# Optimization experiments

Measured on AMD Instinct MI355X. Metric: run time of the kernel, lower is better.

## Reference

```python
import jax, jax.numpy as jnp
import numpy as np

LMAX = 4
S2_DIM = (LMAX + 1) ** 2                                  # 25: s2 irreps, mul 1 per l
SO3_DIM = sum((2 * l + 1) ** 2 for l in range(LMAX + 1))  # 165: so3 irreps, mul 2l+1 per l
B = 2048
F_S2, F_SO3 = 1, 16
N_S2_KERNEL = 48      # s2_healpix_grid(rec_level=1)
N_SO3_KERNEL = 192    # so3_near_identity_grid()
N_ACT_GRID = 4000     # SO3Activation resolution=10, aspect_ratio=2 -> 20x10x20, flattened
N_EVAL = 4608         # so3_healpix_grid(rec_level=2): 192 pixels x 24 gamma


def setup_inputs() -> dict:
    ks = jax.random.split(jax.random.key(0), 7)
    return {
        "x": jax.random.normal(ks[0], (B, F_S2, S2_DIM), jnp.float32),
        "w_s2": jax.random.normal(ks[1], (F_S2, F_SO3, N_S2_KERNEL), jnp.float32),
        "Y": jax.random.normal(ks[2], (N_S2_KERNEL, S2_DIM), jnp.float32),
        "w_so3": jax.random.normal(ks[3], (F_SO3, 1, N_SO3_KERNEL), jnp.float32),
        "D_kernel": jax.random.normal(ks[4], (N_SO3_KERNEL, SO3_DIM), jnp.float32),
        "D_act": jax.random.normal(ks[5], (N_ACT_GRID, SO3_DIM), jnp.float32),
        "eval_wigners": jax.random.normal(ks[6], (SO3_DIM, N_EVAL), jnp.float32) / np.sqrt(SO3_DIM),
    }


def _s2_to_so3_linear(x, psi):
    # e3nn o3.Linear(s2_irreps -> so3_irreps, f_in, f_out, external weights)
    # x:   [B, f_in, 25]  (mul 1 per degree l)
    # psi: [f_in, f_out, 25] ; column l^2+j is the weight to output-multiplicity j of degree l
    f_in, f_out = psi.shape[0], psi.shape[1]
    out, s = [], 0
    for l in range(LMAX + 1):
        d = 2 * l + 1
        x_l = x[..., s:s + d]                       # [B, f_in, d]
        p_l = psi[..., s:s + d]                     # [f_in, f_out, d] (j = out-mul idx)
        o = jnp.einsum('bxm,xyj->byjm', x_l, p_l) / np.sqrt(f_in)
        out.append(o.reshape(x.shape[0], f_out, d * d))
        s += d
    return jnp.concatenate(out, axis=-1)            # [B, f_out, 165]


def _so3_to_so3_linear(x, psi):
    # e3nn o3.Linear(so3_irreps -> so3_irreps, f_in, f_out, external weights)
    # x:   [B, f_in, 165] ; psi: [f_in, f_out, 165]
    f_in, f_out = psi.shape[0], psi.shape[1]
    out, s = [], 0
    for l in range(LMAX + 1):
        d = 2 * l + 1
        x_l = x[..., s:s + d * d].reshape(x.shape[0], f_in, d, d)   # [B,f_in,u,m]
        p_l = psi[..., s:s + d * d].reshape(f_in, f_out, d, d)      # [f_in,f_out,u,v]
        o = jnp.einsum('bxum,xyuv->byvm', x_l, p_l) / np.sqrt(f_in * d)
        out.append(o.reshape(x.shape[0], f_out, d * d))
        s += d * d
    return jnp.concatenate(out, axis=-1)            # [B, f_out, 165]


def _forward(x, w_s2, Y, w_so3, D_kernel, D_act, eval_wigners):
    # --- S2Convolution: kernel = SH-transform of grid weights, then irrep-wise linear
    psi1 = jnp.einsum('ni,xyn->xyi', Y, w_s2) / np.sqrt(N_S2_KERNEL)     # [1,16,25]
    h = _s2_to_so3_linear(x, psi1)                                        # [B,16,165]
    # --- SO3Activation: Fourier -> SO(3) grid -> relu -> Fourier
    g = jnp.einsum('bfi,gi->bfg', h, D_act) / np.sqrt(SO3_DIM)            # [B,16,4000]
    g = jax.nn.relu(g)
    h = jnp.einsum('bfg,gi->bfi', g, D_act) * (np.sqrt(SO3_DIM) / N_ACT_GRID)
    # --- SO3Convolution
    psi2 = jnp.einsum('ni,xyn->xyi', D_kernel, w_so3) / np.sqrt(N_SO3_KERNEL)  # [16,1,165]
    harmonics = _so3_to_so3_linear(h, psi2)                               # [B,1,165]
    # --- compute_probabilities: matmul with eval Wigner-D basis + softmax over grid
    probs = jax.nn.softmax(jnp.einsum('bfi,ie->be', harmonics, eval_wigners), axis=1)  # [B,4608]
    # --- top-k masking: zero out everything below the 5th-highest prob of sample 0
    fifth = jax.lax.top_k(probs, 5)[0][0, 4]
    probs = jnp.where(probs < fifth, 0.0, probs)
    return harmonics, probs


def reference(x, w_s2, Y, w_so3, D_kernel, D_act, eval_wigners):
    return _forward(x, w_s2, Y, w_so3, D_kernel, D_act, eval_wigners)
```

## Files before the change

kernel.cpp:

```cpp
#include <hip/hip_runtime.h>

typedef short bf16x8 __attribute__((ext_vector_type(8)));
typedef float f32x16 __attribute__((ext_vector_type(16)));
typedef int   i32x4  __attribute__((ext_vector_type(4)));

#define INV_SQRT165 0.07784989441615349f
#define FINAL_SCALE 0.0032113081446662823f
#define ZERO16 ((f32x16){0.f,0.f,0.f,0.f,0.f,0.f,0.f,0.f,0.f,0.f,0.f,0.f,0.f,0.f,0.f,0.f})

__device__ __forceinline__ unsigned short f2bf(float f) {
  unsigned int u = __builtin_bit_cast(unsigned int, f);
  unsigned int r = (u + 0x7FFFu + ((u >> 16) & 1u)) >> 16;
  return (unsigned short)r;
}
__device__ __forceinline__ float bf2f(unsigned short h) {
  unsigned int u = ((unsigned int)h) << 16;
  return __builtin_bit_cast(float, u);
}
__device__ __forceinline__ unsigned int pack_bf2(float lo, float hi) {
  return ((unsigned int)f2bf(hi) << 16) | (unsigned int)f2bf(lo);
}

__device__ __forceinline__ void gl_lds16(const void* g, void* l) {
  __builtin_amdgcn_global_load_lds(
      (const __attribute__((address_space(1))) unsigned int*)(unsigned long long)g,
      (__attribute__((address_space(3))) unsigned int*)(unsigned int)(unsigned long long)l,
      16, 0, 0);
}

__device__ __forceinline__ void decode_i(int i, int& lv, int& rel) {
  if (i < 1)       { lv = 0; rel = i; }
  else if (i < 10) { lv = 1; rel = i - 1; }
  else if (i < 35) { lv = 2; rel = i - 10; }
  else if (i < 84) { lv = 3; rel = i - 35; }
  else             { lv = 4; rel = i - 84; }
}
__device__ __forceinline__ int divq(int rel, int lv) {
  const int mag[5] = {32768, 10923, 6554, 4682, 3641};
  return (rel * mag[lv]) >> 15;
}

__device__ __forceinline__ int gperm(int p) {
  int a = p & 3, hlp = (p >> 2) & 1, c = p >> 3;
  return ((c >> 1) << 4) + hlp * 8 + ((c & 1) << 2) + a;
}

__global__ __launch_bounds__(256) void prep_k(const float* __restrict__ Da,
                                              const float* __restrict__ ew,
                                              const float* __restrict__ Y,
                                              const float* __restrict__ w_s2,
                                              const float* __restrict__ Dk,
                                              const float* __restrict__ w_so3,
                                              unsigned short* __restrict__ e1pre,
                                              unsigned short* __restrict__ d2pre,
                                              unsigned short* __restrict__ ewpre,
                                              float* __restrict__ psi2) {
  __shared__ __align__(16) unsigned short lds[13824];
  const int tid = threadIdx.x;
  const int l = tid & 63, hl = l >> 5, ln = l & 31;
  if (blockIdx.x < 128) {
    const int ci = blockIdx.x, g0 = ci * 32;
    float* psi1L = (float*)(lds + 6464);
    for (int e = tid; e < 6400; e += 256) lds[e] = 0;
    for (int e = tid; e < 400; e += 256) {
      int yv = e / 25, iv = e % 25;
      float s = 0.f;
      for (int n = 0; n < 48; n++) s += Y[n * 25 + iv] * w_s2[yv * 48 + n];
      psi1L[e] = s * 0.14433756729740643f;
    }
    __syncthreads();
    int rows = 4000 - g0; if (rows > 32) rows = 32; if (rows < 0) rows = 0;
    int ne = rows * 165;
    for (int e = tid; e < ne; e += 256) {
      int gl_ = e / 165, k = e - gl_ * 165;
      lds[gl_ * 200 + k] = f2bf(Da[g0 * 165 + e]);
    }
    __syncthreads();
#pragma unroll
    for (int it = 0; it < 3; it++) {
      int tt = it * 4 + (tid >> 6);
      int nf = tt >> 1, gk = tt & 1;
      unsigned short v[8];
#pragma unroll
      for (int j = 0; j < 8; j++)
        v[j] = lds[(gk * 16 + hl * 8 + j) * 200 + nf * 32 + ln];
      *(i32x4*)(d2pre + ci * 6144 + tt * 512 + l * 8) = *(i32x4*)v;
    }
    for (int yy = 0; yy < 16; yy++) {
#pragma unroll
      for (int it = 0; it < 4; it++) {
        int idx = it * 256 + tid;
        int kf = idx >> 9, r2 = idx & 511;
        int ll = r2 >> 3, j = r2 & 7;
        int lnn = ll & 31, hll = ll >> 5;
        int k = kf * 16 + hll * 8 + j;
        unsigned short ov = 0;
        if (k < 25) {
          int lv = (k < 1) ? 0 : (k < 4) ? 1 : (k < 9) ? 2 : (k < 16) ? 3 : 4;
          int d = 2 * lv + 1;
          int m = k - lv * lv;
          int off165 = lv * (4 * lv * lv - 1) / 3;
          int gp = gperm(lnn);
          float s = 0.f;
          const float* pr = psi1L + yy * 25 + lv * lv;
          const unsigned short* dr = lds + gp * 200 + off165 + m;
          for (int j2 = 0; j2 < d; j2++) s += pr[j2] * bf2f(dr[j2 * d]);
          ov = f2bf(s * INV_SQRT165);
        }
        e1pre[((yy * 128 + ci) * 2 + kf) * 512 + ll * 8 + j] = ov;
      }
    }
  } else if (blockIdx.x < 200) {
    const int bx2 = blockIdx.x - 128;
    const int n0 = bx2 * 64;
    for (int e = tid; e < 13824; e += 256) lds[e] = 0;
    __syncthreads();
    for (int e = tid; e < 10560; e += 256) {
      int k = e >> 6, n = e & 63;
      lds[k * 72 + n] = f2bf(ew[k * 4608 + n0 + n]);
    }
    __syncthreads();
#pragma unroll
    for (int it = 0; it < 6; it++) {
      int tb = it * 4 + (tid >> 6);
      int nt2 = tb / 12, kf = tb - nt2 * 12;
      unsigned short v[8];
#pragma unroll
      for (int j = 0; j < 8; j++)
        v[j] = lds[(kf * 16 + hl * 8 + j) * 72 + nt2 * 32 + ln];
      *(i32x4*)(ewpre + (bx2 * 2 + nt2) * 6144 + kf * 512 + l * 8) = *(i32x4*)v;
    }
  } else {
    int t = (blockIdx.x - 200) * 256 + tid;
    if (t < 2640) {
      int ch = t / 165, i = t % 165;
      float s = 0.f;
      for (int n = 0; n < 192; n++) s += Dk[n * 165 + i] * w_so3[ch * 192 + n];
      psi2[t] = s * (0.07216878364870323f * FINAL_SCALE);
    }
  }
}

__global__ __launch_bounds__(256, 2) void fused_mlp_k(
    const float* __restrict__ x,
    const unsigned short* __restrict__ e1pre,
    const unsigned short* __restrict__ d2pre,
    unsigned short* __restrict__ part)
{
  __shared__ __align__(16) unsigned char smem[57344];
  const int tid = threadIdx.x;
  const int w = tid >> 6, l = tid & 63;
  const int hl = l >> 5, ln = l & 31;
  const int h = blockIdx.x & 1;
  const int y = (blockIdx.x >> 1) & 15;
  const int btg = blockIdx.x >> 5;
  const int bt = btg * 4 + w;
  const int c0 = h * 64;

  bf16x8 xf[2];
  {
    const float* xr = x + (bt * 32 + ln) * 25;
#pragma unroll
    for (int kf = 0; kf < 2; kf++) {
      unsigned short v[8];
#pragma unroll
      for (int j = 0; j < 8; j++) {
        int k = kf * 16 + hl * 8 + j;
        v[j] = (k < 25) ? f2bf(xr[k]) : (unsigned short)0;
      }
      xf[kf] = *(bf16x8*)v;
    }
  }

  f32x16 o[6];
#pragma unroll
  for (int i = 0; i < 6; i++) o[i] = ZERO16;

  const unsigned short* ebase = e1pre + (y * 128) * 1024;

#pragma unroll
  for (int i = 0; i < 7; i++) {
    int tb = w * 7 + i;
    int cc = (tb >= 14), tb2 = tb - cc * 14;
    const unsigned short* g = (tb2 < 12)
        ? (d2pre + (c0 + cc) * 6144 + tb2 * 512 + l * 8)
        : (ebase + ((c0 + cc) * 2 + (tb2 - 12)) * 512 + l * 8);
    gl_lds16(g, smem + cc * 14336 + tb2 * 1024);
  }

  for (int it = 0; it < 32; it++) {
    __syncthreads();
    const unsigned char* buf = smem + (it & 1) * 28672;
    if (it < 31) {
      unsigned char* nb = smem + ((it + 1) & 1) * 28672;
      const int c = c0 + (it + 1) * 2;
#pragma unroll
      for (int i = 0; i < 7; i++) {
        int tb = w * 7 + i;
        int cc = (tb >= 14), tb2 = tb - cc * 14;
        const unsigned short* g = (tb2 < 12)
            ? (d2pre + (c + cc) * 6144 + tb2 * 512 + l * 8)
            : (ebase + ((c + cc) * 2 + (tb2 - 12)) * 512 + l * 8);
        gl_lds16(g, nb + cc * 14336 + tb2 * 1024);
      }
    }

    bf16x8 a2[2][2];
#pragma unroll
    for (int cc = 0; cc < 2; cc++) {
      const unsigned char* cb = buf + cc * 14336;
      bf16x8 aE0 = *(const bf16x8*)(cb + 12288 + l * 16);
      bf16x8 aE1 = *(const bf16x8*)(cb + 13312 + l * 16);
      f32x16 s = ZERO16;
      s = __builtin_amdgcn_mfma_f32_32x32x16_bf16(aE0, xf[0], s, 0, 0, 0);
      s = __builtin_amdgcn_mfma_f32_32x32x16_bf16(aE1, xf[1], s, 0, 0, 0);
      unsigned int dw[8];
#pragma unroll
      for (int p = 0; p < 8; p++)
        dw[p] = pack_bf2(fmaxf(s[2 * p], 0.f), fmaxf(s[2 * p + 1], 0.f));
      i32x4 q0 = (i32x4){(int)dw[0], (int)dw[1], (int)dw[2], (int)dw[3]};
      i32x4 q1 = (i32x4){(int)dw[4], (int)dw[5], (int)dw[6], (int)dw[7]};
      a2[cc][0] = __builtin_bit_cast(bf16x8, q0);
      a2[cc][1] = __builtin_bit_cast(bf16x8, q1);
    }

#pragma unroll
    for (int cc = 0; cc < 2; cc++) {
      const unsigned char* cb = buf + cc * 14336;
#pragma unroll
      for (int gk = 0; gk < 2; gk++) {
#pragma unroll
        for (int nf = 0; nf < 6; nf++) {
          bf16x8 b2 = *(const bf16x8*)(cb + (nf * 2 + gk) * 1024 + l * 16);
          o[nf] = __builtin_amdgcn_mfma_f32_32x32x16_bf16(a2[cc][gk], b2, o[nf], 0, 0, 0);
        }
      }
    }
  }

  unsigned short* pp = part + (size_t)((h * 16 + y) * 2048 + bt * 32) * 192;
#pragma unroll
  for (int nf = 0; nf < 6; nf++) {
    int n = nf * 32 + ln;
    if (n < 176) {
#pragma unroll
      for (int r = 0; r < 16; r++) {
        int row = (r & 3) + 8 * (r >> 2) + 4 * hl;
        pp[row * 192 + n] = f2bf(o[nf][r]);
      }
    }
  }
}

__global__ __launch_bounds__(256) void so3_k(const unsigned short* __restrict__ part,
                                             const float* __restrict__ psi2,
                                             float* __restrict__ harm_out,
                                             unsigned short* __restrict__ harmbpre) {
  __shared__ float lds[4 * 16 * 180];
  const int tid = threadIdx.x;
  const int b0 = blockIdx.x * 4;
  {
    const int ybl = tid >> 2;
    const int yy = ybl & 15, bloc = ybl >> 4;
    const int s = tid & 3;
    const unsigned int* r0 = (const unsigned int*)(part + ((size_t)(0 * 16 + yy) * 2048 + b0 + bloc) * 192);
    const unsigned int* r1 = (const unsigned int*)(part + ((size_t)(1 * 16 + yy) * 2048 + b0 + bloc) * 192);
    float* dst = lds + (bloc * 16 + yy) * 180;
#pragma unroll
    for (int t = 0; t < 22; t++) {
      int d = s * 22 + t;
      if (d < 88) {
        unsigned int u0 = r0[d], u1 = r1[d];
        int n0 = d * 2;
        dst[n0]     = bf2f((unsigned short)(u0 & 0xFFFF)) + bf2f((unsigned short)(u1 & 0xFFFF));
        dst[n0 + 1] = bf2f((unsigned short)(u0 >> 16))    + bf2f((unsigned short)(u1 >> 16));
      }
    }
  }
  __syncthreads();
  for (int jj = tid; jj < 768; jj += 256) {
    int e = (jj * 683) >> 17;
    int i = jj - e * 192;
    int bb = b0 + e;
    unsigned short* hb = harmbpre + (((bb >> 5) * 12 + (i >> 4)) << 9)
                       + ((i >> 3) & 1) * 256 + (bb & 31) * 8 + (i & 7);
    if (i < 165) {
      const float* row0 = lds + e * (16 * 180);
      int lv, rel; decode_i(i, lv, rel);
      int d = 2 * lv + 1;
      int off = i - rel;
      int v = divq(rel, lv), m = rel - v * d;
      float s = 0.f;
      for (int ch = 0; ch < 16; ch++) {
        const float* rw = row0 + ch * 180 + off;
        const float* p2 = psi2 + ch * 165 + off;
        for (int u = 0; u < d; u++) s += rw[u * d + m] * p2[u * d + v];
      }
      s *= 0.25f * rsqrtf((float)d);
      harm_out[bb * 165 + i] = s;
      *hb = f2bf(s);
    } else {
      *hb = 0;
    }
  }
}

__global__ __launch_bounds__(64) void eval_k(
    const unsigned short* __restrict__ harmbpre,
    const unsigned short* __restrict__ ewpre,
    float* __restrict__ logits)
{
  const int l = threadIdx.x;
  const int hl = l >> 5, ln = l & 31;
  const int mt = blockIdx.y;
  const int n0 = blockIdx.x * 192;

  bf16x8 a[12];
  const short* ap = (const short*)harmbpre + mt * 6144 + l * 8;
#pragma unroll
  for (int kf = 0; kf < 12; kf++) a[kf] = *(const bf16x8*)(ap + kf * 512);

  f32x16 acc[6];
#pragma unroll
  for (int nf = 0; nf < 6; nf++) acc[nf] = ZERO16;

  const short* bp = (const short*)ewpre + (blockIdx.x * 6) * 6144 + l * 8;
#pragma unroll
  for (int kf = 0; kf < 12; kf++) {
#pragma unroll
    for (int nf = 0; nf < 6; nf++) {
      bf16x8 b = *(const bf16x8*)(bp + nf * 6144 + kf * 512);
      acc[nf] = __builtin_amdgcn_mfma_f32_32x32x16_bf16(a[kf], b, acc[nf], 0, 0, 0);
    }
  }
#pragma unroll
  for (int nf = 0; nf < 6; nf++) {
    const int col = n0 + nf * 32 + ln;
#pragma unroll
    for (int r = 0; r < 16; r++) {
      int row = (r & 3) + 8 * (r >> 2) + 4 * hl;
      logits[(mt * 32 + row) * 4608 + col] = acc[nf][r];
    }
  }
}

__global__ __launch_bounds__(256) void fifth_k(const float* __restrict__ logit0,
                                               float* __restrict__ fifth) {
  __shared__ float buf[4608];
  __shared__ float sm[4], ss[4];
  __shared__ float wv[4]; __shared__ int wi[4];
  __shared__ float gbest;
  const int tid = threadIdx.x;
  const int l = tid & 63, w = tid >> 6;
  float v[18];
  float mx = -3.4e38f;
#pragma unroll
  for (int i = 0; i < 18; i++) {
    v[i] = logit0[i * 256 + tid];
    buf[i * 256 + tid] = v[i];
    mx = fmaxf(mx, v[i]);
  }
#pragma unroll
  for (int off = 32; off >= 1; off >>= 1) mx = fmaxf(mx, __shfl_xor(mx, off));
  if (l == 0) sm[w] = mx;
  __syncthreads();
  mx = fmaxf(fmaxf(sm[0], sm[1]), fmaxf(sm[2], sm[3]));
  float s = 0.f;
#pragma unroll
  for (int i = 0; i < 18; i++) { v[i] = __expf(v[i] - mx); s += v[i]; }
#pragma unroll
  for (int off = 32; off >= 1; off >>= 1) s += __shfl_xor(s, off);
  if (l == 0) ss[w] = s;
  __syncthreads();
  s = ss[0] + ss[1] + ss[2] + ss[3];
  float inv = 1.f / s;

  float ff = 0.f;
  for (int it = 0; it < 5; it++) {
    float bm = -3.4e38f; int bi = 0;
    for (int i = tid; i < 4608; i += 256) {
      float xx = buf[i];
      if (xx > bm) { bm = xx; bi = i; }
    }
    for (int off = 32; off >= 1; off >>= 1) {
      float ov = __shfl_xor(bm, off); int oi = __shfl_xor(bi, off);
      if (ov > bm) { bm = ov; bi = oi; }
    }
    if (l == 0) { wv[w] = bm; wi[w] = bi; }
    __syncthreads();
    if (tid == 0) {
      float B = wv[0]; int I = wi[0];
      for (int k = 1; k < 4; k++) if (wv[k] > B) { B = wv[k]; I = wi[k]; }
      gbest = B;
      buf[I] = -3.4e38f;
    }
    __syncthreads();
    ff = gbest;
    __syncthreads();
  }
  if (tid == 0) *fifth = __expf(ff - mx) * inv;
}

__global__ __launch_bounds__(256) void smthresh_k(float* __restrict__ probs,
                                                  const float* __restrict__ fifth) {
  float* p = probs + (size_t)blockIdx.x * 4608;
  const int tid = threadIdx.x;
  const int l = tid & 63, w = tid >> 6;
  __shared__ float sm[4], ss[4];
  float v[18];
  float mx = -3.4e38f;
#pragma unroll
  for (int i = 0; i < 18; i++) { v[i] = p[i * 256 + tid]; mx = fmaxf(mx, v[i]); }
#pragma unroll
  for (int off = 32; off >= 1; off >>= 1) mx = fmaxf(mx, __shfl_xor(mx, off));
  if (l == 0) sm[w] = mx;
  __syncthreads();
  mx = fmaxf(fmaxf(sm[0], sm[1]), fmaxf(sm[2], sm[3]));
  float s = 0.f;
#pragma unroll
  for (int i = 0; i < 18; i++) { v[i] = __expf(v[i] - mx); s += v[i]; }
#pragma unroll
  for (int off = 32; off >= 1; off >>= 1) s += __shfl_xor(s, off);
  if (l == 0) ss[w] = s;
  __syncthreads();
  s = ss[0] + ss[1] + ss[2] + ss[3];
  float inv = 1.f / s;
  float t = *fifth;
#pragma unroll
  for (int i = 0; i < 18; i++) {
    float pv = v[i] * inv;
    p[i * 256 + tid] = (pv < t) ? 0.f : pv;
  }
}

extern "C" void kernel_launch(void* const* d_in, const int* in_sizes, int n_in,
                              void* d_out, int out_size, void* d_ws, size_t ws_size,
                              hipStream_t stream) {
  const float* x     = (const float*)d_in[0];
  const float* w_s2  = (const float*)d_in[1];
  const float* Y     = (const float*)d_in[2];
  const float* w_so3 = (const float*)d_in[3];
  const float* Dk    = (const float*)d_in[4];
  const float* Da    = (const float*)d_in[5];
  const float* ew    = (const float*)d_in[6];

  float* out = (float*)d_out;
  float* harm_out = out;
  float* probs    = out + 337920;
  unsigned short* part = (unsigned short*)probs;

  char* ws = (char*)d_ws;
  float* psi2  = (float*)(ws + 0);
  float* fifth = (float*)(ws + 10560);
  unsigned short* e1pre    = (unsigned short*)(ws + 12288);
  unsigned short* d2pre    = (unsigned short*)(ws + 4206592);
  unsigned short* ewpre    = (unsigned short*)(ws + 5779456);
  unsigned short* harmbpre = (unsigned short*)(ws + 7548928);

  prep_k<<<211, 256, 0, stream>>>(Da, ew, Y, w_s2, Dk, w_so3, e1pre, d2pre, ewpre, psi2);
  fused_mlp_k<<<512, 256, 0, stream>>>(x, e1pre, d2pre, part);
  so3_k<<<512, 256, 0, stream>>>(part, psi2, harm_out, harmbpre);
  eval_k<<<dim3(24, 64), 64, 0, stream>>>(harmbpre, ewpre, probs);
  fifth_k<<<1, 256, 0, stream>>>(probs, fifth);
  smthresh_k<<<2048, 256, 0, stream>>>(probs, fifth);
}
```

Measured before the change: 234.9 us.

## Retile MLP warps over two batch tiles, fuse top-k into softmax, cache psi2

```diff
diff --git a/kernel.cpp b/kernel.cpp
--- a/kernel.cpp
+++ b/kernel.cpp
@@ -17,8 +17,10 @@
   unsigned int u = ((unsigned int)h) << 16;
   return __builtin_bit_cast(float, u);
 }
-__device__ __forceinline__ unsigned int pack_bf2(float lo, float hi) {
-  return ((unsigned int)f2bf(hi) << 16) | (unsigned int)f2bf(lo);
+__device__ __forceinline__ unsigned int pack_bf2f(float lo, float hi) {
+  unsigned int a = (__builtin_bit_cast(unsigned int, lo) + 0x8000u) >> 16;
+  unsigned int b = (__builtin_bit_cast(unsigned int, hi) + 0x8000u) & 0xFFFF0000u;
+  return b | a;
 }
 
 __device__ __forceinline__ void gl_lds16(const void* g, void* l) {
@@ -154,12 +156,13 @@
   const int h = blockIdx.x & 1;
   const int y = (blockIdx.x >> 1) & 15;
   const int btg = blockIdx.x >> 5;
-  const int bt = btg * 4 + w;
+  const int bw = w >> 1, ng = w & 1;
   const int c0 = h * 64;
 
-  bf16x8 xf[2];
-  {
-    const float* xr = x + (bt * 32 + ln) * 25;
+  bf16x8 xf[2][2];
+#pragma unroll
+  for (int t = 0; t < 2; t++) {
+    const float* xr = x + (btg * 128 + bw * 64 + t * 32 + ln) * 25;
 #pragma unroll
     for (int kf = 0; kf < 2; kf++) {
       unsigned short v[8];
@@ -168,7 +171,7 @@
         int k = kf * 16 + hl * 8 + j;
         v[j] = (k < 25) ? f2bf(xr[k]) : (unsigned short)0;
       }
-      xf[kf] = *(bf16x8*)v;
+      xf[t][kf] = *(bf16x8*)v;
     }
   }
 
@@ -205,48 +208,55 @@
       }
     }
 
-    bf16x8 a2[2][2];
 #pragma unroll
     for (int cc = 0; cc < 2; cc++) {
       const unsigned char* cb = buf + cc * 14336;
       bf16x8 aE0 = *(const bf16x8*)(cb + 12288 + l * 16);
       bf16x8 aE1 = *(const bf16x8*)(cb + 13312 + l * 16);
-      f32x16 s = ZERO16;
-      s = __builtin_amdgcn_mfma_f32_32x32x16_bf16(aE0, xf[0], s, 0, 0, 0);
-      s = __builtin_amdgcn_mfma_f32_32x32x16_bf16(aE1, xf[1], s, 0, 0, 0);
-      unsigned int dw[8];
-#pragma unroll
-      for (int p = 0; p < 8; p++)
-        dw[p] = pack_bf2(fmaxf(s[2 * p], 0.f), fmaxf(s[2 * p + 1], 0.f));
-      i32x4 q0 = (i32x4){(int)dw[0], (int)dw[1], (int)dw[2], (int)dw[3]};
-      i32x4 q1 = (i32x4){(int)dw[4], (int)dw[5], (int)dw[6], (int)dw[7]};
-      a2[cc][0] = __builtin_bit_cast(bf16x8, q0);
-      a2[cc][1] = __builtin_bit_cast(bf16x8, q1);
-    }
-
-#pragma unroll
-    for (int cc = 0; cc < 2; cc++) {
-      const unsigned char* cb = buf + cc * 14336;
+      f32x16 s0 = ZERO16, s1 = ZERO16;
+      s0 = __builtin_amdgcn_mfma_f32_32x32x16_bf16(aE0, xf[0][0], s0, 0, 0, 0);
+      s1 = __builtin_amdgcn_mfma_f32_32x32x16_bf16(aE0, xf[1][0], s1, 0, 0, 0);
+      s0 = __builtin_amdgcn_mfma_f32_32x32x16_bf16(aE1, xf[0][1], s0, 0, 0, 0);
+      s1 = __builtin_amdgcn_mfma_f32_32x32x16_bf16(aE1, xf[1][1], s1, 0, 0, 0);
+
+      bf16x8 a2[2][2];
+#pragma unroll
+      for (int t = 0; t < 2; t++) {
+        const f32x16& sv = t ? s1 : s0;
+        unsigned int dw[8];
+#pragma unroll
+        for (int p = 0; p < 8; p++)
+          dw[p] = pack_bf2f(fmaxf(sv[2 * p], 0.f), fmaxf(sv[2 * p + 1], 0.f));
+        i32x4 q0 = (i32x4){(int)dw[0], (int)dw[1], (int)dw[2], (int)dw[3]};
+        i32x4 q1 = (i32x4){(int)dw[4], (int)dw[5], (int)dw[6], (int)dw[7]};
+        a2[t][0] = __builtin_bit_cast(bf16x8, q0);
+        a2[t][1] = __builtin_bit_cast(bf16x8, q1);
+      }
+
 #pragma unroll
       for (int gk = 0; gk < 2; gk++) {
 #pragma unroll
-        for (int nf = 0; nf < 6; nf++) {
-          bf16x8 b2 = *(const bf16x8*)(cb + (nf * 2 + gk) * 1024 + l * 16);
-          o[nf] = __builtin_amdgcn_mfma_f32_32x32x16_bf16(a2[cc][gk], b2, o[nf], 0, 0, 0);
+        for (int nf = 0; nf < 3; nf++) {
+          bf16x8 b2 = *(const bf16x8*)(cb + ((ng * 3 + nf) * 2 + gk) * 1024 + l * 16);
+          o[nf]     = __builtin_amdgcn_mfma_f32_32x32x16_bf16(a2[0][gk], b2, o[nf],     0, 0, 0);
+          o[3 + nf] = __builtin_amdgcn_mfma_f32_32x32x16_bf16(a2[1][gk], b2, o[3 + nf], 0, 0, 0);
         }
       }
     }
   }
 
-  unsigned short* pp = part + (size_t)((h * 16 + y) * 2048 + bt * 32) * 192;
-#pragma unroll
-  for (int nf = 0; nf < 6; nf++) {
-    int n = nf * 32 + ln;
-    if (n < 176) {
-#pragma unroll
-      for (int r = 0; r < 16; r++) {
-        int row = (r & 3) + 8 * (r >> 2) + 4 * hl;
-        pp[row * 192 + n] = f2bf(o[nf][r]);
+#pragma unroll
+  for (int t = 0; t < 2; t++) {
+    unsigned short* pp = part + (size_t)((h * 16 + y) * 2048 + btg * 128 + bw * 64 + t * 32) * 192;
+#pragma unroll
+    for (int nf = 0; nf < 3; nf++) {
+      int n = ng * 96 + nf * 32 + ln;
+      if (n < 176) {
+#pragma unroll
+        for (int r = 0; r < 16; r++) {
+          int row = (r & 3) + 8 * (r >> 2) + 4 * hl;
+          pp[row * 192 + n] = f2bf(o[t * 3 + nf][r]);
+        }
       }
     }
   }
@@ -257,8 +267,10 @@
                                              float* __restrict__ harm_out,
                                              unsigned short* __restrict__ harmbpre) {
   __shared__ float lds[4 * 16 * 180];
+  __shared__ float p2s[2640];
   const int tid = threadIdx.x;
   const int b0 = blockIdx.x * 4;
+  for (int e = tid; e < 2640; e += 256) p2s[e] = psi2[e];
   {
     const int ybl = tid >> 2;
     const int yy = ybl & 15, bloc = ybl >> 4;
@@ -293,7 +305,7 @@
       float s = 0.f;
       for (int ch = 0; ch < 16; ch++) {
         const float* rw = row0 + ch * 180 + off;
-        const float* p2 = psi2 + ch * 165 + off;
+        const float* p2 = p2s + ch * 165 + off;
         for (int u = 0; u < d; u++) s += rw[u * d + m] * p2[u * d + v];
       }
       s *= 0.25f * rsqrtf((float)d);
@@ -308,7 +320,8 @@
 __global__ __launch_bounds__(64) void eval_k(
     const unsigned short* __restrict__ harmbpre,
     const unsigned short* __restrict__ ewpre,
-    float* __restrict__ logits)
+    float* __restrict__ logits,
+    float* __restrict__ logit0)
 {
   const int l = threadIdx.x;
   const int hl = l >> 5, ln = l & 31;
@@ -342,38 +355,53 @@
       logits[(mt * 32 + row) * 4608 + col] = acc[nf][r];
     }
   }
-}
-
-__global__ __launch_bounds__(256) void fifth_k(const float* __restrict__ logit0,
-                                               float* __restrict__ fifth) {
+  if (mt == 0 && hl == 0) {
+#pragma unroll
+    for (int nf = 0; nf < 6; nf++) logit0[n0 + nf * 32 + ln] = acc[nf][0];
+  }
+}
+
+__global__ __launch_bounds__(256) void smthresh_k(float* __restrict__ probs,
+                                                  const float* __restrict__ logit0) {
   __shared__ float buf[4608];
-  __shared__ float sm[4], ss[4];
+  __shared__ float sm[8], ss[8];
   __shared__ float wv[4]; __shared__ int wi[4];
   __shared__ float gbest;
+  float* p = probs + (size_t)blockIdx.x * 4608;
   const int tid = threadIdx.x;
   const int l = tid & 63, w = tid >> 6;
   float v[18];
-  float mx = -3.4e38f;
+  float mx = -3.4e38f, mx0 = -3.4e38f;
 #pragma unroll
   for (int i = 0; i < 18; i++) {
-    v[i] = logit0[i * 256 + tid];
-    buf[i * 256 + tid] = v[i];
+    v[i] = p[i * 256 + tid];
+    float t0 = logit0[i * 256 + tid];
+    buf[i * 256 + tid] = t0;
     mx = fmaxf(mx, v[i]);
-  }
-#pragma unroll
-  for (int off = 32; off >= 1; off >>= 1) mx = fmaxf(mx, __shfl_xor(mx, off));
-  if (l == 0) sm[w] = mx;
+    mx0 = fmaxf(mx0, t0);
+  }
+#pragma unroll
+  for (int off = 32; off >= 1; off >>= 1) {
+    mx = fmaxf(mx, __shfl_xor(mx, off));
+    mx0 = fmaxf(mx0, __shfl_xor(mx0, off));
+  }
+  if (l == 0) { sm[w] = mx; sm[4 + w] = mx0; }
   __syncthreads();
-  mx = fmaxf(fmaxf(sm[0], sm[1]), fmaxf(sm[2], sm[3]));
-  float s = 0.f;
-#pragma unroll
-  for (int i = 0; i < 18; i++) { v[i] = __expf(v[i] - mx); s += v[i]; }
-#pragma unroll
-  for (int off = 32; off >= 1; off >>= 1) s += __shfl_xor(s, off);
-  if (l == 0) ss[w] = s;
+  mx  = fmaxf(fmaxf(sm[0], sm[1]), fmaxf(sm[2], sm[3]));
+  mx0 = fmaxf(fmaxf(sm[4], sm[5]), fmaxf(sm[6], sm[7]));
+  float s = 0.f, s0 = 0.f;
+#pragma unroll
+  for (int i = 0; i < 18; i++) {
+    v[i] = __expf(v[i] - mx); s += v[i];
+    s0 += __expf(buf[i * 256 + tid] - mx0);
+  }
+#pragma unroll
+  for (int off = 32; off >= 1; off >>= 1) { s += __shfl_xor(s, off); s0 += __shfl_xor(s0, off); }
+  if (l == 0) { ss[w] = s; ss[4 + w] = s0; }
   __syncthreads();
-  s = ss[0] + ss[1] + ss[2] + ss[3];
-  float inv = 1.f / s;
+  s  = ss[0] + ss[1] + ss[2] + ss[3];
+  s0 = ss[4] + ss[5] + ss[6] + ss[7];
+  float inv = 1.f / s, inv0 = 1.f / s0;
 
   float ff = 0.f;
   for (int it = 0; it < 5; it++) {
@@ -398,34 +426,7 @@
     ff = gbest;
     __syncthreads();
   }
-  if (tid == 0) *fifth = __expf(ff - mx) * inv;
-}
-
-__global__ __launch_bounds__(256) void smthresh_k(float* __restrict__ probs,
-                                                  const float* __restrict__ fifth) {
-  float* p = probs + (size_t)blockIdx.x * 4608;
-  const int tid = threadIdx.x;
-  const int l = tid & 63, w = tid >> 6;
-  __shared__ float sm[4], ss[4];
-  float v[18];
-  float mx = -3.4e38f;
-#pragma unroll
-  for (int i = 0; i < 18; i++) { v[i] = p[i * 256 + tid]; mx = fmaxf(mx, v[i]); }
-#pragma unroll
-  for (int off = 32; off >= 1; off >>= 1) mx = fmaxf(mx, __shfl_xor(mx, off));
-  if (l == 0) sm[w] = mx;
-  __syncthreads();
-  mx = fmaxf(fmaxf(sm[0], sm[1]), fmaxf(sm[2], sm[3]));
-  float s = 0.f;
-#pragma unroll
-  for (int i = 0; i < 18; i++) { v[i] = __expf(v[i] - mx); s += v[i]; }
-#pragma unroll
-  for (int off = 32; off >= 1; off >>= 1) s += __shfl_xor(s, off);
-  if (l == 0) ss[w] = s;
-  __syncthreads();
-  s = ss[0] + ss[1] + ss[2] + ss[3];
-  float inv = 1.f / s;
-  float t = *fifth;
+  float t = __expf(ff - mx0) * inv0;
 #pragma unroll
   for (int i = 0; i < 18; i++) {
     float pv = v[i] * inv;
@@ -451,16 +452,15 @@
 
   char* ws = (char*)d_ws;
   float* psi2  = (float*)(ws + 0);
-  float* fifth = (float*)(ws + 10560);
   unsigned short* e1pre    = (unsigned short*)(ws + 12288);
   unsigned short* d2pre    = (unsigned short*)(ws + 4206592);
   unsigned short* ewpre    = (unsigned short*)(ws + 5779456);
   unsigned short* harmbpre = (unsigned short*)(ws + 7548928);
+  float* logit0 = (float*)(ws + 8335360);
 
   prep_k<<<211, 256, 0, stream>>>(Da, ew, Y, w_s2, Dk, w_so3, e1pre, d2pre, ewpre, psi2);
   fused_mlp_k<<<512, 256, 0, stream>>>(x, e1pre, d2pre, part);
   so3_k<<<512, 256, 0, stream>>>(part, psi2, harm_out, harmbpre);
-  eval_k<<<dim3(24, 64), 64, 0, stream>>>(harmbpre, ewpre, probs);
-  fifth_k<<<1, 256, 0, stream>>>(probs, fifth);
-  smthresh_k<<<2048, 256, 0, stream>>>(probs, fifth);
-}
+  eval_k<<<dim3(24, 64), 64, 0, stream>>>(harmbpre, ewpre, probs, logit0);
+  smthresh_k<<<2048, 256, 0, stream>>>(probs, logit0);
+}
```

Result: slower. 245.0 us (+4.3%).

## Split prep and MLP work across more blocks, shrink LDS, cache psi2, add logit0 buffer

Applied to the files above, without the earlier changes.

```diff
diff --git a/kernel.cpp b/kernel.cpp
--- a/kernel.cpp
+++ b/kernel.cpp
@@ -17,8 +17,10 @@
   unsigned int u = ((unsigned int)h) << 16;
   return __builtin_bit_cast(float, u);
 }
-__device__ __forceinline__ unsigned int pack_bf2(float lo, float hi) {
-  return ((unsigned int)f2bf(hi) << 16) | (unsigned int)f2bf(lo);
+__device__ __forceinline__ unsigned int pack_bf2f(float lo, float hi) {
+  unsigned int a = (__builtin_bit_cast(unsigned int, lo) + 0x8000u) >> 16;
+  unsigned int b = (__builtin_bit_cast(unsigned int, hi) + 0x8000u) & 0xFFFF0000u;
+  return b | a;
 }
 
 __device__ __forceinline__ void gl_lds16(const void* g, void* l) {
@@ -58,8 +60,9 @@
   __shared__ __align__(16) unsigned short lds[13824];
   const int tid = threadIdx.x;
   const int l = tid & 63, hl = l >> 5, ln = l & 31;
-  if (blockIdx.x < 128) {
-    const int ci = blockIdx.x, g0 = ci * 32;
+  if (blockIdx.x < 512) {
+    const int ci = blockIdx.x >> 2, yg = blockIdx.x & 3;
+    const int g0 = ci * 32;
     float* psi1L = (float*)(lds + 6464);
     for (int e = tid; e < 6400; e += 256) lds[e] = 0;
     for (int e = tid; e < 400; e += 256) {
@@ -76,17 +79,20 @@
       lds[gl_ * 200 + k] = f2bf(Da[g0 * 165 + e]);
     }
     __syncthreads();
-#pragma unroll
-    for (int it = 0; it < 3; it++) {
-      int tt = it * 4 + (tid >> 6);
-      int nf = tt >> 1, gk = tt & 1;
-      unsigned short v[8];
-#pragma unroll
-      for (int j = 0; j < 8; j++)
-        v[j] = lds[(gk * 16 + hl * 8 + j) * 200 + nf * 32 + ln];
-      *(i32x4*)(d2pre + ci * 6144 + tt * 512 + l * 8) = *(i32x4*)v;
-    }
-    for (int yy = 0; yy < 16; yy++) {
+    if (yg == 0) {
+#pragma unroll
+      for (int it = 0; it < 3; it++) {
+        int tt = it * 4 + (tid >> 6);
+        int nf = tt >> 1, gk = tt & 1;
+        unsigned short v[8];
+#pragma unroll
+        for (int j = 0; j < 8; j++)
+          v[j] = lds[(gk * 16 + hl * 8 + j) * 200 + nf * 32 + ln];
+        *(i32x4*)(d2pre + ci * 6144 + tt * 512 + l * 8) = *(i32x4*)v;
+      }
+    }
+    for (int yi = 0; yi < 4; yi++) {
+      int yy = yg * 4 + yi;
 #pragma unroll
       for (int it = 0; it < 4; it++) {
         int idx = it * 256 + tid;
@@ -110,8 +116,8 @@
         e1pre[((yy * 128 + ci) * 2 + kf) * 512 + ll * 8 + j] = ov;
       }
     }
-  } else if (blockIdx.x < 200) {
-    const int bx2 = blockIdx.x - 128;
+  } else if (blockIdx.x < 584) {
+    const int bx2 = blockIdx.x - 512;
     const int n0 = bx2 * 64;
     for (int e = tid; e < 13824; e += 256) lds[e] = 0;
     __syncthreads();
@@ -131,7 +137,7 @@
       *(i32x4*)(ewpre + (bx2 * 2 + nt2) * 6144 + kf * 512 + l * 8) = *(i32x4*)v;
     }
   } else {
-    int t = (blockIdx.x - 200) * 256 + tid;
+    int t = (blockIdx.x - 584) * 256 + tid;
     if (t < 2640) {
       int ch = t / 165, i = t % 165;
       float s = 0.f;
@@ -141,20 +147,21 @@
   }
 }
 
-__global__ __launch_bounds__(256, 2) void fused_mlp_k(
+__global__ __launch_bounds__(256, 4) void fused_mlp_k(
     const float* __restrict__ x,
     const unsigned short* __restrict__ e1pre,
     const unsigned short* __restrict__ d2pre,
     unsigned short* __restrict__ part)
 {
-  __shared__ __align__(16) unsigned char smem[57344];
+  __shared__ __align__(16) unsigned char smem[28672];
   const int tid = threadIdx.x;
   const int w = tid >> 6, l = tid & 63;
   const int hl = l >> 5, ln = l & 31;
   const int h = blockIdx.x & 1;
   const int y = (blockIdx.x >> 1) & 15;
   const int btg = blockIdx.x >> 5;
-  const int bt = btg * 4 + w;
+  const int bw = w >> 1, ng = w & 1;
+  const int bt = btg * 2 + bw;
   const int c0 = h * 64;
 
   bf16x8 xf[2];
@@ -172,76 +179,66 @@
     }
   }
 
-  f32x16 o[6];
-#pragma unroll
-  for (int i = 0; i < 6; i++) o[i] = ZERO16;
+  f32x16 o[3];
+#pragma unroll
+  for (int i = 0; i < 3; i++) o[i] = ZERO16;
 
   const unsigned short* ebase = e1pre + (y * 128) * 1024;
 
 #pragma unroll
-  for (int i = 0; i < 7; i++) {
-    int tb = w * 7 + i;
-    int cc = (tb >= 14), tb2 = tb - cc * 14;
-    const unsigned short* g = (tb2 < 12)
-        ? (d2pre + (c0 + cc) * 6144 + tb2 * 512 + l * 8)
-        : (ebase + ((c0 + cc) * 2 + (tb2 - 12)) * 512 + l * 8);
-    gl_lds16(g, smem + cc * 14336 + tb2 * 1024);
-  }
-
-  for (int it = 0; it < 32; it++) {
-    __syncthreads();
-    const unsigned char* buf = smem + (it & 1) * 28672;
-    if (it < 31) {
-      unsigned char* nb = smem + ((it + 1) & 1) * 28672;
-      const int c = c0 + (it + 1) * 2;
-#pragma unroll
-      for (int i = 0; i < 7; i++) {
-        int tb = w * 7 + i;
-        int cc = (tb >= 14), tb2 = tb - cc * 14;
-        const unsigned short* g = (tb2 < 12)
-            ? (d2pre + (c + cc) * 6144 + tb2 * 512 + l * 8)
-            : (ebase + ((c + cc) * 2 + (tb2 - 12)) * 512 + l * 8);
-        gl_lds16(g, nb + cc * 14336 + tb2 * 1024);
-      }
-    }
-
-    bf16x8 a2[2][2];
-#pragma unroll
-    for (int cc = 0; cc < 2; cc++) {
-      const unsigned char* cb = buf + cc * 14336;
-      bf16x8 aE0 = *(const bf16x8*)(cb + 12288 + l * 16);
-      bf16x8 aE1 = *(const bf16x8*)(cb + 13312 + l * 16);
-      f32x16 s = ZERO16;
-      s = __builtin_amdgcn_mfma_f32_32x32x16_bf16(aE0, xf[0], s, 0, 0, 0);
-      s = __builtin_amdgcn_mfma_f32_32x32x16_bf16(aE1, xf[1], s, 0, 0, 0);
-      unsigned int dw[8];
-#pragma unroll
-      for (int p = 0; p < 8; p++)
-        dw[p] = pack_bf2(fmaxf(s[2 * p], 0.f), fmaxf(s[2 * p + 1], 0.f));
-      i32x4 q0 = (i32x4){(int)dw[0], (int)dw[1], (int)dw[2], (int)dw[3]};
-      i32x4 q1 = (i32x4){(int)dw[4], (int)dw[5], (int)dw[6], (int)dw[7]};
-      a2[cc][0] = __builtin_bit_cast(bf16x8, q0);
-      a2[cc][1] = __builtin_bit_cast(bf16x8, q1);
-    }
-
-#pragma unroll
-    for (int cc = 0; cc < 2; cc++) {
-      const unsigned char* cb = buf + cc * 14336;
-#pragma unroll
-      for (int gk = 0; gk < 2; gk++) {
-#pragma unroll
-        for (int nf = 0; nf < 6; nf++) {
-          bf16x8 b2 = *(const bf16x8*)(cb + (nf * 2 + gk) * 1024 + l * 16);
-          o[nf] = __builtin_amdgcn_mfma_f32_32x32x16_bf16(a2[cc][gk], b2, o[nf], 0, 0, 0);
+  for (int i = 0; i < 4; i++) {
+    int tb = w * 4 + i;
+    if (tb < 14) {
+      const unsigned short* g = (tb < 12) ? (d2pre + c0 * 6144 + tb * 512 + l * 8)
+                                          : (ebase + (c0 * 2 + (tb - 12)) * 512 + l * 8);
+      gl_lds16(g, smem + tb * 1024);
+    }
+  }
+
+  for (int ci = 0; ci < 64; ci++) {
+    __syncthreads();
+    const unsigned char* cb = smem + (ci & 1) * 14336;
+    if (ci < 63) {
+      unsigned char* nb = smem + ((ci + 1) & 1) * 14336;
+      const int c = c0 + ci + 1;
+#pragma unroll
+      for (int i = 0; i < 4; i++) {
+        int tb = w * 4 + i;
+        if (tb < 14) {
+          const unsigned short* g = (tb < 12) ? (d2pre + c * 6144 + tb * 512 + l * 8)
+                                              : (ebase + (c * 2 + (tb - 12)) * 512 + l * 8);
+          gl_lds16(g, nb + tb * 1024);
         }
       }
     }
+    bf16x8 aE0 = *(const bf16x8*)(cb + 12288 + l * 16);
+    bf16x8 aE1 = *(const bf16x8*)(cb + 13312 + l * 16);
+    f32x16 s = ZERO16;
+    s = __builtin_amdgcn_mfma_f32_32x32x16_bf16(aE0, xf[0], s, 0, 0, 0);
+    s = __builtin_amdgcn_mfma_f32_32x32x16_bf16(aE1, xf[1], s, 0, 0, 0);
+    unsigned int dw[8];
+#pragma unroll
+    for (int p = 0; p < 8; p++)
+      dw[p] = pack_bf2f(fmaxf(s[2 * p], 0.f), fmaxf(s[2 * p + 1], 0.f));
+    i32x4 q0 = (i32x4){(int)dw[0], (int)dw[1], (int)dw[2], (int)dw[3]};
+    i32x4 q1 = (i32x4){(int)dw[4], (int)dw[5], (int)dw[6], (int)dw[7]};
+    bf16x8 a20 = __builtin_bit_cast(bf16x8, q0);
+    bf16x8 a21 = __builtin_bit_cast(bf16x8, q1);
+#pragma unroll
+    for (int gk = 0; gk < 2; gk++) {
+      bf16x8 a2 = gk ? a21 : a20;
+#pragma unroll
+      for (int nf = 0; nf < 3; nf++) {
+        bf16x8 b2 = *(const bf16x8*)(cb + ((ng * 3 + nf) * 2 + gk) * 1024 + l * 16);
+        o[nf] = __builtin_amdgcn_mfma_f32_32x32x16_bf16(a2, b2, o[nf], 0, 0, 0);
+      }
+    }
   }
 
   unsigned short* pp = part + (size_t)((h * 16 + y) * 2048 + bt * 32) * 192;
 #pragma unroll
-  for (int nf = 0; nf < 6; nf++) {
-    int n = nf * 32 + ln;
+  for (int nf = 0; nf < 3; nf++) {
+    int n = ng * 96 + nf * 32 + ln;
     if (n < 176) {
 #pragma unroll
       for (int r = 0; r < 16; r++) {
@@ -257,8 +254,10 @@
                                              float* __restrict__ harm_out,
                                              unsigned short* __restrict__ harmbpre) {
   __shared__ float lds[4 * 16 * 180];
+  __shared__ float p2s[2640];
   const int tid = threadIdx.x;
   const int b0 = blockIdx.x * 4;
+  for (int e = tid; e < 2640; e += 256) p2s[e] = psi2[e];
   {
     const int ybl = tid >> 2;
     const int yy = ybl & 15, bloc = ybl >> 4;
@@ -293,7 +292,7 @@
       float s = 0.f;
       for (int ch = 0; ch < 16; ch++) {
         const float* rw = row0 + ch * 180 + off;
-        const float* p2 = psi2 + ch * 165 + off;
+        const float* p2 = p2s + ch * 165 + off;
         for (int u = 0; u < d; u++) s += rw[u * d + m] * p2[u * d + v];
       }
       s *= 0.25f * rsqrtf((float)d);
@@ -308,7 +307,8 @@
 __global__ __launch_bounds__(64) void eval_k(
     const unsigned short* __restrict__ harmbpre,
     const unsigned short* __restrict__ ewpre,
-    float* __restrict__ logits)
+    float* __restrict__ logits,
+    float* __restrict__ logit0)
 {
   const int l = threadIdx.x;
   const int hl = l >> 5, ln = l & 31;
@@ -341,6 +341,10 @@
       int row = (r & 3) + 8 * (r >> 2) + 4 * hl;
       logits[(mt * 32 + row) * 4608 + col] = acc[nf][r];
     }
+  }
+  if (mt == 0 && hl == 0) {
+#pragma unroll
+    for (int nf = 0; nf < 6; nf++) logit0[n0 + nf * 32 + ln] = acc[nf][0];
   }
 }
 
@@ -367,7 +371,7 @@
   mx = fmaxf(fmaxf(sm[0], sm[1]), fmaxf(sm[2], sm[3]));
   float s = 0.f;
 #pragma unroll
-  for (int i = 0; i < 18; i++) { v[i] = __expf(v[i] - mx); s += v[i]; }
+  for (int i = 0; i < 18; i++) s += __expf(v[i] - mx);
 #pragma unroll
   for (int off = 32; off >= 1; off >>= 1) s += __shfl_xor(s, off);
   if (l == 0) ss[w] = s;
@@ -456,11 +460,12 @@
   unsigned short* d2pre    = (unsigned short*)(ws + 4206592);
   unsigned short* ewpre    = (unsigned short*)(ws + 5779456);
   unsigned short* harmbpre = (unsigned short*)(ws + 7548928);
-
-  prep_k<<<211, 256, 0, stream>>>(Da, ew, Y, w_s2, Dk, w_so3, e1pre, d2pre, ewpre, psi2);
-  fused_mlp_k<<<512, 256, 0, stream>>>(x, e1pre, d2pre, part);
+  float* logit0 = (float*)(ws + 8335360);
+
+  prep_k<<<595, 256, 0, stream>>>(Da, ew, Y, w_s2, Dk, w_so3, e1pre, d2pre, ewpre, psi2);
+  fused_mlp_k<<<1024, 256, 0, stream>>>(x, e1pre, d2pre, part);
   so3_k<<<512, 256, 0, stream>>>(part, psi2, harm_out, harmbpre);
-  eval_k<<<dim3(24, 64), 64, 0, stream>>>(harmbpre, ewpre, probs);
-  fifth_k<<<1, 256, 0, stream>>>(probs, fifth);
+  eval_k<<<dim3(24, 64), 64, 0, stream>>>(harmbpre, ewpre, probs, logit0);
+  fifth_k<<<1, 256, 0, stream>>>(logit0, fifth);
   smthresh_k<<<2048, 256, 0, stream>>>(probs, fifth);
 }
```

New measurement: 238.5 us. No clear change (+1.6%).
